# Kernel tuning notes

Measured on AMD Instinct MI355X. Metric: run time of the kernel, lower is better.

Reference implementation:

```python
import jax, jax.numpy as jnp
import numpy as np

B, T, S = 4, 128, 8192
HID, NH, NKV, HD = 2560, 8, 4, 256
INTER = 10240
WINDOW = 1024
SOFTCAP = 50.0
SCALING = 256 ** -0.5  # query_pre_attn_scalar ** -0.5
EPS = 1e-6
NEG = -2.3819763e38  # large negative for masking (matches Gemma mask value)
ROPE_THETA = 10000.0


def _rmsnorm(x, w):
    xf = x.astype(jnp.float32)
    o = xf * jax.lax.rsqrt(jnp.mean(xf * xf, axis=-1, keepdims=True) + EPS)
    return (o * (1.0 + w.astype(jnp.float32))).astype(x.dtype)


def _rope(x, cos, sin):
    # split-half rotation, matching torch apply_rotary_emb (chunk->complex->mul)
    d2 = x.shape[-1] // 2
    x1, x2 = x[..., :d2], x[..., d2:]
    c = cos[None, :, None, :]  # [1,T,1,D/2]
    s = sin[None, :, None, :]
    return jnp.concatenate([x1 * c - x2 * s, x1 * s + x2 * c], axis=-1)


def setup_inputs() -> dict:
    key = jax.random.key(0)
    ks = jax.random.split(key, 14)
    hidden_states = jax.random.normal(ks[0], (B, T, HID), jnp.float32)
    kv_write_indices = jnp.arange(T, dtype=jnp.int32)
    k_cache = jnp.zeros((B, S, NKV, HD), jnp.float32)
    v_cache = jnp.zeros((B, S, NKV, HD), jnp.float32)
    # rotary tables for positions 0..T-1
    inv = 1.0 / (ROPE_THETA ** (np.arange(0, HD, 2)[: HD // 2].astype(np.float32) / HD))
    fr = np.outer(np.arange(T, dtype=np.float32), inv).astype(np.float32)
    freqs_cos = jnp.asarray(np.cos(fr))
    freqs_sin = jnp.asarray(np.sin(fr))
    # masks: query i sits at absolute position i; cache slots >= T are unwritten
    qpos = jnp.arange(T)[:, None]
    kpos = jnp.arange(S)[None, :]
    causal = kpos <= qpos
    local = causal & ((qpos - kpos) < WINDOW)
    mask = jnp.broadcast_to(jnp.where(causal, 0.0, NEG)[None, None], (B, 1, T, S)).astype(jnp.float32)
    local_mask = jnp.broadcast_to(jnp.where(local, 0.0, NEG)[None, None], (B, 1, T, S)).astype(jnp.float32)
    sc = 0.02
    w_qkv = sc * jax.random.normal(ks[1], ((NH + 2 * NKV) * HD, HID), jnp.float32)
    w_o = sc * jax.random.normal(ks[2], (HID, NH * HD), jnp.float32)
    q_norm_w = 0.1 * jax.random.normal(ks[3], (HD,), jnp.float32)
    k_norm_w = 0.1 * jax.random.normal(ks[4], (HD,), jnp.float32)
    in_ln_w = 0.1 * jax.random.normal(ks[5], (HID,), jnp.float32)
    post_attn_ln_w = 0.1 * jax.random.normal(ks[6], (HID,), jnp.float32)
    pre_ffw_ln_w = 0.1 * jax.random.normal(ks[7], (HID,), jnp.float32)
    post_ffw_ln_w = 0.1 * jax.random.normal(ks[8], (HID,), jnp.float32)
    w_gate = sc * jax.random.normal(ks[9], (INTER, HID), jnp.float32)
    w_up = sc * jax.random.normal(ks[10], (INTER, HID), jnp.float32)
    w_down = sc * jax.random.normal(ks[11], (HID, INTER), jnp.float32)
    return {
        "hidden_states": hidden_states, "freqs_cos": freqs_cos, "freqs_sin": freqs_sin,
        "kv_write_indices": kv_write_indices, "k_cache": k_cache, "v_cache": v_cache,
        "mask": mask, "local_mask": local_mask,
        "w_qkv": w_qkv, "w_o": w_o, "q_norm_w": q_norm_w, "k_norm_w": k_norm_w,
        "in_ln_w": in_ln_w, "post_attn_ln_w": post_attn_ln_w,
        "pre_ffw_ln_w": pre_ffw_ln_w, "post_ffw_ln_w": post_ffw_ln_w,
        "w_gate": w_gate, "w_up": w_up, "w_down": w_down,
    }


def reference(hidden_states, freqs_cos, freqs_sin, kv_write_indices, k_cache, v_cache,
              mask, local_mask, w_qkv, w_o, q_norm_w, k_norm_w, in_ln_w,
              post_attn_ln_w, pre_ffw_ln_w, post_ffw_ln_w, w_gate, w_up, w_down):
    b, t, _ = hidden_states.shape
    residual = hidden_states
    h = _rmsnorm(hidden_states, in_ln_w)
    qkv = h @ w_qkv.T
    q_sz, kv_sz = NH * HD, NKV * HD
    xq = qkv[..., :q_sz].reshape(b, t, NH, HD)
    xk = qkv[..., q_sz:q_sz + kv_sz].reshape(b, t, NKV, HD)
    xv = qkv[..., q_sz + kv_sz:].reshape(b, t, NKV, HD)
    xq = _rmsnorm(xq, q_norm_w)  # QK-norm
    xk = _rmsnorm(xk, k_norm_w)
    xq = _rope(xq, freqs_cos, freqs_sin)
    xk = _rope(xk, freqs_cos, freqs_sin)
    kc = k_cache.at[:, kv_write_indices].set(xk)  # index_copy_ on dim 1
    vc = v_cache.at[:, kv_write_indices].set(xv)
    g = NH // NKV
    q = (xq * SCALING).reshape(b, t, NKV, g, HD)
    # GQA without repeat_interleave: group dim g shares each kv head
    scores = jnp.einsum('btkgd,bskd->bkgts', q, kc)
    scores = SOFTCAP * jnp.tanh(scores / SOFTCAP)  # logit softcapping
    scores = scores + local_mask[:, :, None]  # LOCAL_SLIDING -> use local mask
    probs = jax.nn.softmax(scores.astype(jnp.float32), axis=-1).astype(q.dtype)
    attn = jnp.einsum('bkgts,bskd->btkgd', probs, vc).reshape(b, t, NH * HD)
    attn = attn @ w_o.T
    h = residual + _rmsnorm(attn, post_attn_ln_w)
    residual = h
    x = _rmsnorm(h, pre_ffw_ln_w)
    gate = jax.nn.gelu(x @ w_gate.T, approximate=True)
    mlp = (gate * (x @ w_up.T)) @ w_down.T
    return residual + _rmsnorm(mlp, post_ffw_ln_w)
```

## Files before the change

### kernel.cpp

```cpp
#include <hip/hip_runtime.h>
#include <hip/hip_bf16.h>

#define B_ 4
#define T_ 128
#define HID 2560
#define NH 8
#define NKV 4
#define HD 256
#define INTER 10240
#define MROWS 512
#define EPS 1e-6f

typedef float f32x4 __attribute__((ext_vector_type(4)));
typedef __bf16 bf16x8 __attribute__((ext_vector_type(8)));

__device__ __forceinline__ unsigned short f2bf(float f){
  unsigned int u = __builtin_bit_cast(unsigned int, f);
  u += 0x7fffu + ((u >> 16) & 1u);
  return (unsigned short)(u >> 16);
}
__device__ __forceinline__ float bf2f(unsigned short u){
  unsigned int x = ((unsigned int)u) << 16;
  return __builtin_bit_cast(float, x);
}
__device__ __forceinline__ unsigned int cvtpk(float lo, float hi){
  unsigned int r;
  asm("v_cvt_pk_bf16_f32 %0, %1, %2" : "=v"(r) : "v"(lo), "v"(hi));
  return r;
}

__device__ __forceinline__ float bsum256(float v, float* buf){
  #pragma unroll
  for (int o = 32; o; o >>= 1) v += __shfl_xor(v, o);
  __syncthreads();
  if ((threadIdx.x & 63) == 0) buf[threadIdx.x >> 6] = v;
  __syncthreads();
  return buf[0] + buf[1] + buf[2] + buf[3];
}

__global__ __launch_bounds__(256) void rms_in(
    const float* __restrict__ x, const float* __restrict__ w,
    unsigned short* __restrict__ out)
{
  __shared__ float buf[4];
  const int r = blockIdx.x, tid = threadIdx.x;
  const float* xp = x + (size_t)r * HID;
  float v[10]; float ss = 0.f;
  #pragma unroll
  for (int j = 0; j < 10; j++){ v[j] = xp[tid + j*256]; ss += v[j]*v[j]; }
  ss = bsum256(ss, buf);
  float s = rsqrtf(ss * (1.f/HID) + EPS);
  #pragma unroll
  for (int j = 0; j < 10; j++){
    int i = tid + j*256;
    out[(size_t)r*HID + i] = f2bf(v[j] * s * (1.f + w[i]));
  }
}

template<bool BF16OUT>
__global__ __launch_bounds__(256, 2) void gemm_big(
    const unsigned short* __restrict__ A,
    const float* __restrict__ B0,
    const float* __restrict__ B1,
    int n_hi,
    void* __restrict__ Cv,
    int N, int K, int klen)
{
  __shared__ char As[2][256*64];
  __shared__ char Bs[2][128*64];
  const int tid = threadIdx.x;
  const int bid = (blockIdx.x & 7) * ((int)gridDim.x >> 3) + (blockIdx.x >> 3);
  const int bm = (bid & 1) << 8;
  const int bn = (bid >> 1) << 7;
  const int k0 = blockIdx.y * klen;
  const int nt = klen >> 5;

  const int srow = tid >> 1, shalf = tid & 1;
  const size_t A128 = (size_t)128 * K;
  const unsigned short* ApG = A + (size_t)(bm + srow) * K + k0 + (shalf << 4);
  const float* Bb = (bn < n_hi) ? B0 : B1;
  const int bnr = (bn < n_hi) ? bn : (bn - n_hi);
  const float* BpG = Bb + (size_t)(bnr + srow) * K + k0 + (shalf << 4);

  const int wave = tid >> 6, lane = tid & 63;
  const int wm = (wave & 1) << 7;
  const int wn = (wave >> 1) << 6;
  const int fr = lane & 15, kq = lane >> 4;
  const int aslot = ((kq ^ ((fr >> 1) & 3)) << 4);
  const int arsw = (srow >> 1) & 3;
  const int s0 = (((2*shalf)     ^ arsw) << 4);
  const int s1 = (((2*shalf + 1) ^ arsw) << 4);

  f32x4 acc[8][4];
  #pragma unroll
  for (int i = 0; i < 8; i++)
    #pragma unroll
    for (int j = 0; j < 4; j++)
      #pragma unroll
      for (int e = 0; e < 4; e++) acc[i][j][e] = 0.f;

  uint4 ra0, ra1, ra2, ra3; float4 rb0, rb1, rb2, rb3;
  uint4 sa0, sa1, sa2, sa3; float4 sb0, sb1, sb2, sb3;

#define LOAD_R(tt) { const unsigned short* ap = ApG + ((tt) << 5); const float* bp = BpG + ((tt) << 5); \
  ra0 = *(const uint4*)(ap); ra1 = *(const uint4*)(ap + 8); \
  ra2 = *(const uint4*)(ap + A128); ra3 = *(const uint4*)(ap + A128 + 8); \
  rb0 = *(const float4*)(bp); rb1 = *(const float4*)(bp + 4); \
  rb2 = *(const float4*)(bp + 8); rb3 = *(const float4*)(bp + 12); }
#define LOAD_S(tt) { const unsigned short* ap = ApG + ((tt) << 5); const float* bp = BpG + ((tt) << 5); \
  sa0 = *(const uint4*)(ap); sa1 = *(const uint4*)(ap + 8); \
  sa2 = *(const uint4*)(ap + A128); sa3 = *(const uint4*)(ap + A128 + 8); \
  sb0 = *(const float4*)(bp); sb1 = *(const float4*)(bp + 4); \
  sb2 = *(const float4*)(bp + 8); sb3 = *(const float4*)(bp + 12); }
#define WRITE_TILE(cur, a0,a1,a2,a3, b0,b1,b2,b3) { \
  char* abase = &As[cur][srow*64]; \
  *(uint4*)(abase + s0) = a0; \
  *(uint4*)(abase + s1) = a1; \
  *(uint4*)(abase + 128*64 + s0) = a2; \
  *(uint4*)(abase + 128*64 + s1) = a3; \
  uint4 w0, w1; \
  w0.x = cvtpk(b0.x,b0.y); w0.y = cvtpk(b0.z,b0.w); \
  w0.z = cvtpk(b1.x,b1.y); w0.w = cvtpk(b1.z,b1.w); \
  w1.x = cvtpk(b2.x,b2.y); w1.y = cvtpk(b2.z,b2.w); \
  w1.z = cvtpk(b3.x,b3.y); w1.w = cvtpk(b3.z,b3.w); \
  char* bbase = &Bs[cur][srow*64]; \
  *(uint4*)(bbase + s0) = w0; \
  *(uint4*)(bbase + s1) = w1; }

  auto COMPUTE = [&](int cur){
    const char* ab = As[cur];
    const char* bb = Bs[cur];
    bf16x8 af[8], bfv[4];
    #pragma unroll
    for (int mi = 0; mi < 8; mi++)
      af[mi] = *(const bf16x8*)(ab + ((wm + mi*16 + fr) << 6) + aslot);
    #pragma unroll
    for (int ni = 0; ni < 4; ni++)
      bfv[ni] = *(const bf16x8*)(bb + ((wn + ni*16 + fr) << 6) + aslot);
    __builtin_amdgcn_s_setprio(1);
    #pragma unroll
    for (int mi = 0; mi < 8; mi++)
      #pragma unroll
      for (int ni = 0; ni < 4; ni++)
        acc[mi][ni] = __builtin_amdgcn_mfma_f32_16x16x32_bf16(af[mi], bfv[ni], acc[mi][ni], 0, 0, 0);
    __builtin_amdgcn_s_setprio(0);
  };

  LOAD_R(0);
  LOAD_S(1);
  for (int t = 0; t < nt; t += 2) {
    WRITE_TILE(0, ra0,ra1,ra2,ra3, rb0,rb1,rb2,rb3);
    __syncthreads();
    if (t + 2 < nt) LOAD_R(t + 2);
    COMPUTE(0);
    WRITE_TILE(1, sa0,sa1,sa2,sa3, sb0,sb1,sb2,sb3);
    __syncthreads();
    if (t + 3 < nt) LOAD_S(t + 3);
    COMPUTE(1);
  }
#undef LOAD_R
#undef LOAD_S
#undef WRITE_TILE

  #pragma unroll
  for (int mi = 0; mi < 8; mi++) {
    #pragma unroll
    for (int ni = 0; ni < 4; ni++) {
      int m = bm + wm + mi*16 + kq*4;
      int n = bn + wn + ni*16 + fr;
      if (BF16OUT) {
        unsigned short* Cp = (unsigned short*)Cv + (size_t)blockIdx.y * MROWS * N;
        #pragma unroll
        for (int i = 0; i < 4; i++)
          Cp[(size_t)(m + i) * N + n] = f2bf(acc[mi][ni][i]);
      } else {
        float* Cp = (float*)Cv + (size_t)blockIdx.y * MROWS * N;
        #pragma unroll
        for (int i = 0; i < 4; i++)
          Cp[(size_t)(m + i) * N + n] = acc[mi][ni][i];
      }
    }
  }
}

__global__ __launch_bounds__(64) void qkv_post(
    const float* __restrict__ qkvp,
    const float* __restrict__ fcos, const float* __restrict__ fsin,
    const float* __restrict__ qnw, const float* __restrict__ knw,
    float* __restrict__ qout, float* __restrict__ kT, float* __restrict__ vout)
{
  const int row = blockIdx.x;
  const int hh  = blockIdx.y;
  const int b = row >> 7, t = row & 127;
  const int l = threadIdx.x;
  const size_t MS = (size_t)MROWS * 4096;
  const float* src = qkvp + (size_t)row * 4096 + hh * 256;
  float x[4];
  #pragma unroll
  for (int j = 0; j < 4; j++){
    int d = l + j*64;
    x[j] = src[d] + src[d + MS] + src[d + 2*MS] + src[d + 3*MS];
  }
  if (hh >= 12) {
    float* vp = vout + ((size_t)(b*NKV + (hh-12)) * T_ + t) * HD;
    #pragma unroll
    for (int j = 0; j < 4; j++) vp[l + j*64] = x[j];
    return;
  }
  float ss = x[0]*x[0] + x[1]*x[1] + x[2]*x[2] + x[3]*x[3];
  #pragma unroll
  for (int o = 32; o; o >>= 1) ss += __shfl_xor(ss, o);
  float r = rsqrtf(ss * (1.f/HD) + EPS);
  const float* nw = (hh < 8) ? qnw : knw;
  #pragma unroll
  for (int j = 0; j < 4; j++){ int d = l + j*64; x[j] = x[j] * r * (1.f + nw[d]); }
  float c0 = fcos[t*128 + l],      s0 = fsin[t*128 + l];
  float c1 = fcos[t*128 + l + 64], s1 = fsin[t*128 + l + 64];
  float y0 = x[0]*c0 - x[2]*s0;
  float y2 = x[0]*s0 + x[2]*c0;
  float y1 = x[1]*c1 - x[3]*s1;
  float y3 = x[1]*s1 + x[3]*c1;
  if (hh < 8) {
    float* qp = qout + ((size_t)(b*NH + hh) * T_ + t) * HD;
    const float sc = 0.0625f;
    qp[l] = y0*sc; qp[l+64] = y1*sc; qp[l+128] = y2*sc; qp[l+192] = y3*sc;
  } else {
    float* kp = kT + (size_t)(b*NKV + (hh-8)) * HD * T_;
    kp[(size_t)(l)*T_ + t] = y0;  kp[(size_t)(l+64)*T_ + t] = y1;
    kp[(size_t)(l+128)*T_ + t] = y2; kp[(size_t)(l+192)*T_ + t] = y3;
  }
}

__global__ __launch_bounds__(128) void attn_fwd(
    const float* __restrict__ q, const float* __restrict__ kT,
    const float* __restrict__ V, unsigned short* __restrict__ attn_out)
{
  const int id = blockIdx.x;
  const int t = id & 127;
  const int h = (id >> 7) & 7;
  const int b = id >> 10;
  const int kvh = h >> 1;
  const int tid = threadIdx.x;
  __shared__ float qs[256];
  __shared__ float sc[128];
  __shared__ float red[128];
  const float* qp = q + (size_t)id * HD;
  qs[tid] = qp[tid]; qs[tid + 128] = qp[tid + 128];
  __syncthreads();
  const float* kp = kT + (size_t)(b*NKV + kvh) * HD * T_;
  float dot = 0.f;
  const bool valid = (tid <= t);
  if (valid) {
    #pragma unroll 8
    for (int d = 0; d < 256; d++) dot += qs[d] * kp[(size_t)d*T_ + tid];
  }
  float score = valid ? 50.f * tanhf(dot * 0.02f) : -3.0e38f;
  sc[tid] = score; red[tid] = score;
  __syncthreads();
  for (int o = 64; o; o >>= 1){ if (tid < o) red[tid] = fmaxf(red[tid], red[tid+o]); __syncthreads(); }
  float m = red[0];
  __syncthreads();
  float p = valid ? __expf(score - m) : 0.f;
  sc[tid] = p; red[tid] = p;
  __syncthreads();
  for (int o = 64; o; o >>= 1){ if (tid < o) red[tid] += red[tid+o]; __syncthreads(); }
  float inv = 1.f / red[0];
  const float* vp = V + (size_t)(b*NKV + kvh) * T_ * HD;
  float a0 = 0.f, a1 = 0.f;
  for (int s = 0; s <= t; s++){
    float ps = sc[s];
    a0 += ps * vp[(size_t)s*HD + tid];
    a1 += ps * vp[(size_t)s*HD + tid + 128];
  }
  size_t orow = ((size_t)(b*T_ + t)) * 2048 + h * 256;
  attn_out[orow + tid]       = f2bf(a0 * inv);
  attn_out[orow + tid + 128] = f2bf(a1 * inv);
}

__global__ __launch_bounds__(256) void post_attn_k(
    const float* __restrict__ op, const float* __restrict__ hs,
    const float* __restrict__ wpost, const float* __restrict__ wpre,
    float* __restrict__ h2, unsigned short* __restrict__ xout)
{
  __shared__ float buf[4];
  const int r = blockIdx.x, tid = threadIdx.x;
  const size_t MS = (size_t)MROWS * HID;
  float o[10]; float ss = 0.f;
  #pragma unroll
  for (int j = 0; j < 10; j++){
    size_t i = (size_t)r*HID + tid + j*256;
    float v = 0.f;
    #pragma unroll
    for (int s = 0; s < 8; s++) v += op[i + s*MS];
    o[j] = v; ss += v*v;
  }
  ss = bsum256(ss, buf);
  float s = rsqrtf(ss*(1.f/HID) + EPS);
  float h[10]; float s2 = 0.f;
  #pragma unroll
  for (int j = 0; j < 10; j++){
    int i = tid + j*256;
    float hv = hs[(size_t)r*HID + i] + o[j]*s*(1.f + wpost[i]);
    h[j] = hv; h2[(size_t)r*HID + i] = hv; s2 += hv*hv;
  }
  s2 = bsum256(s2, buf);
  float sc2 = rsqrtf(s2*(1.f/HID) + EPS);
  #pragma unroll
  for (int j = 0; j < 10; j++){
    int i = tid + j*256;
    xout[(size_t)r*HID + i] = f2bf(h[j]*sc2*(1.f + wpre[i]));
  }
}

__global__ __launch_bounds__(256) void act_fuse(
    const unsigned short* __restrict__ gu,
    unsigned short* __restrict__ act)
{
  const int r = blockIdx.x;
  const size_t MS = (size_t)MROWS * 20480;
  const unsigned short* rowp = gu + (size_t)r * 20480;
  for (int c = threadIdx.x; c < INTER; c += 256){
    float g = 0.f, u = 0.f;
    #pragma unroll
    for (int s = 0; s < 4; s++){
      g += bf2f(rowp[s*MS + c]);
      u += bf2f(rowp[s*MS + c + INTER]);
    }
    float tt = tanhf(0.7978845608f * (g + 0.044715f * g*g*g));
    float ge = 0.5f * g * (1.f + tt);
    act[(size_t)r*INTER + c] = f2bf(ge * u);
  }
}

__global__ __launch_bounds__(256) void final_k(
    const float* __restrict__ dp, const float* __restrict__ h2,
    const float* __restrict__ w, float* __restrict__ out)
{
  __shared__ float buf[4];
  const int r = blockIdx.x, tid = threadIdx.x;
  const size_t MS = (size_t)MROWS * HID;
  float m[10]; float ss = 0.f;
  #pragma unroll
  for (int j = 0; j < 10; j++){
    size_t i = (size_t)r*HID + tid + j*256;
    float v = 0.f;
    #pragma unroll
    for (int s = 0; s < 8; s++) v += dp[i + s*MS];
    m[j] = v; ss += v*v;
  }
  ss = bsum256(ss, buf);
  float s = rsqrtf(ss*(1.f/HID) + EPS);
  #pragma unroll
  for (int j = 0; j < 10; j++){
    int i = tid + j*256;
    out[(size_t)r*HID + i] = h2[(size_t)r*HID + i] + m[j]*s*(1.f + w[i]);
  }
}

extern "C" void kernel_launch(void* const* d_in, const int* in_sizes, int n_in,
                              void* d_out, int out_size, void* d_ws, size_t ws_size,
                              hipStream_t stream)
{
  const float* hs     = (const float*)d_in[0];
  const float* fcos   = (const float*)d_in[1];
  const float* fsin   = (const float*)d_in[2];
  const float* w_qkv  = (const float*)d_in[8];
  const float* w_o    = (const float*)d_in[9];
  const float* qnw    = (const float*)d_in[10];
  const float* knw    = (const float*)d_in[11];
  const float* in_ln  = (const float*)d_in[12];
  const float* w_post = (const float*)d_in[13];
  const float* w_pre  = (const float*)d_in[14];
  const float* w_pffw = (const float*)d_in[15];
  const float* w_gate = (const float*)d_in[16];
  const float* w_up   = (const float*)d_in[17];
  const float* w_down = (const float*)d_in[18];
  float* out = (float*)d_out;

  char* p = (char*)d_ws;
  auto alloc = [&](size_t bytes)->void*{ void* r = p; p += (bytes + 255) & ~(size_t)255; return r; };
  void* P0 = alloc((size_t)4*MROWS*20480*2);
  void* P1 = alloc((size_t)8*MROWS*HID*4);
  unsigned short* h_b   = (unsigned short*)alloc((size_t)MROWS*HID*2);
  float* qbuf           = (float*)alloc((size_t)B_*NH*T_*HD*4);
  float* kT             = (float*)alloc((size_t)B_*NKV*HD*T_*4);
  float* vbuf           = (float*)alloc((size_t)B_*NKV*T_*HD*4);
  unsigned short* att_b = (unsigned short*)alloc((size_t)MROWS*2048*2);
  float* h2             = (float*)alloc((size_t)MROWS*HID*4);
  unsigned short* x_b   = (unsigned short*)alloc((size_t)MROWS*HID*2);
  unsigned short* act_b = (unsigned short*)alloc((size_t)MROWS*INTER*2);

  float* qkv_p          = (float*)P0;
  unsigned short* gu_p  = (unsigned short*)P0;
  float* o_p            = (float*)P1;
  float* down_p         = (float*)P1;

  rms_in<<<MROWS, 256, 0, stream>>>(hs, in_ln, h_b);
  gemm_big<false><<<dim3(64, 4), 256, 0, stream>>>(h_b, w_qkv, w_qkv, 1<<30, qkv_p, 4096, 2560, 640);
  qkv_post<<<dim3(MROWS, 16), 64, 0, stream>>>(qkv_p, fcos, fsin, qnw, knw, qbuf, kT, vbuf);
  attn_fwd<<<B_*NH*T_, 128, 0, stream>>>(qbuf, kT, vbuf, att_b);
  gemm_big<false><<<dim3(40, 8), 256, 0, stream>>>(att_b, w_o, w_o, 1<<30, o_p, 2560, 2048, 256);
  post_attn_k<<<MROWS, 256, 0, stream>>>(o_p, hs, w_post, w_pre, h2, x_b);
  gemm_big<true><<<dim3(320, 4), 256, 0, stream>>>(x_b, w_gate, w_up, 10240, gu_p, 20480, 2560, 640);
  act_fuse<<<MROWS, 256, 0, stream>>>(gu_p, act_b);
  gemm_big<false><<<dim3(40, 8), 256, 0, stream>>>(act_b, w_down, w_down, 1<<30, down_p, 2560, 10240, 1280);
  final_k<<<MROWS, 256, 0, stream>>>(down_p, h2, w_pffw, out);
}
```

Before: 369.7 us.

## Pre-tile activations into K-blocked layout and load A fragments directly to registers

Producers (rms_in, attn_fwd, post_attn_k, act_fuse) now write bf16 activations in a K-chunked [K/32][512][32] layout. The GEMM loads A fragments straight from global memory into registers, skipping the LDS staging and LDS reads for A; only B still goes through shared memory. Split-K counts are doubled for the QKV, O and down projections, and the reduction kernels and workspace grow to match. This adds more global A traffic per wave (no LDS reuse across waves) and more partial-sum reduction work in exchange for lower LDS pressure and higher grid parallelism.

```diff
diff --git a/kernel.cpp b/kernel.cpp
--- a/kernel.cpp
+++ b/kernel.cpp
@@ -38,6 +38,7 @@
   return buf[0] + buf[1] + buf[2] + buf[3];
 }
 
+
 __global__ __launch_bounds__(256) void rms_in(
     const float* __restrict__ x, const float* __restrict__ w,
     unsigned short* __restrict__ out)
@@ -53,43 +54,42 @@
   #pragma unroll
   for (int j = 0; j < 10; j++){
     int i = tid + j*256;
-    out[(size_t)r*HID + i] = f2bf(v[j] * s * (1.f + w[i]));
+    out[((size_t)(i >> 5) * MROWS + r) * 32 + (i & 31)] = f2bf(v[j] * s * (1.f + w[i]));
   }
 }
 
 template<bool BF16OUT>
 __global__ __launch_bounds__(256, 2) void gemm_big(
-    const unsigned short* __restrict__ A,
+    const unsigned short* __restrict__ Ap,
     const float* __restrict__ B0,
     const float* __restrict__ B1,
     int n_hi,
     void* __restrict__ Cv,
     int N, int K, int klen)
 {
-  __shared__ char As[2][256*64];
   __shared__ char Bs[2][128*64];
   const int tid = threadIdx.x;
   const int bid = (blockIdx.x & 7) * ((int)gridDim.x >> 3) + (blockIdx.x >> 3);
   const int bm = (bid & 1) << 8;
   const int bn = (bid >> 1) << 7;
-  const int k0 = blockIdx.y * klen;
+  const int kt0 = (blockIdx.y * klen) >> 5;
   const int nt = klen >> 5;
 
   const int srow = tid >> 1, shalf = tid & 1;
-  const size_t A128 = (size_t)128 * K;
-  const unsigned short* ApG = A + (size_t)(bm + srow) * K + k0 + (shalf << 4);
   const float* Bb = (bn < n_hi) ? B0 : B1;
   const int bnr = (bn < n_hi) ? bn : (bn - n_hi);
-  const float* BpG = Bb + (size_t)(bnr + srow) * K + k0 + (shalf << 4);
+  const float* BpG = Bb + (size_t)(bnr + srow) * K + (kt0 << 5) + (shalf << 4);
 
   const int wave = tid >> 6, lane = tid & 63;
   const int wm = (wave & 1) << 7;
   const int wn = (wave >> 1) << 6;
   const int fr = lane & 15, kq = lane >> 4;
-  const int aslot = ((kq ^ ((fr >> 1) & 3)) << 4);
-  const int arsw = (srow >> 1) & 3;
-  const int s0 = (((2*shalf)     ^ arsw) << 4);
-  const int s1 = (((2*shalf + 1) ^ arsw) << 4);
+  const int bslot = ((kq ^ ((fr >> 1) & 3)) << 4);
+  const int brsw = (srow >> 1) & 3;
+  const int s0 = (((2*shalf)     ^ brsw) << 4);
+  const int s1 = (((2*shalf + 1) ^ brsw) << 4);
+
+  const unsigned short* ApL = Ap + ((size_t)kt0 * MROWS + bm + wm + fr) * 32 + kq * 8;
 
   f32x4 acc[8][4];
   #pragma unroll
@@ -99,26 +99,18 @@
       #pragma unroll
       for (int e = 0; e < 4; e++) acc[i][j][e] = 0.f;
 
-  uint4 ra0, ra1, ra2, ra3; float4 rb0, rb1, rb2, rb3;
-  uint4 sa0, sa1, sa2, sa3; float4 sb0, sb1, sb2, sb3;
-
-#define LOAD_R(tt) { const unsigned short* ap = ApG + ((tt) << 5); const float* bp = BpG + ((tt) << 5); \
-  ra0 = *(const uint4*)(ap); ra1 = *(const uint4*)(ap + 8); \
-  ra2 = *(const uint4*)(ap + A128); ra3 = *(const uint4*)(ap + A128 + 8); \
-  rb0 = *(const float4*)(bp); rb1 = *(const float4*)(bp + 4); \
-  rb2 = *(const float4*)(bp + 8); rb3 = *(const float4*)(bp + 12); }
-#define LOAD_S(tt) { const unsigned short* ap = ApG + ((tt) << 5); const float* bp = BpG + ((tt) << 5); \
-  sa0 = *(const uint4*)(ap); sa1 = *(const uint4*)(ap + 8); \
-  sa2 = *(const uint4*)(ap + A128); sa3 = *(const uint4*)(ap + A128 + 8); \
-  sb0 = *(const float4*)(bp); sb1 = *(const float4*)(bp + 4); \
-  sb2 = *(const float4*)(bp + 8); sb3 = *(const float4*)(bp + 12); }
-#define WRITE_TILE(cur, a0,a1,a2,a3, b0,b1,b2,b3) { \
-  char* abase = &As[cur][srow*64]; \
-  *(uint4*)(abase + s0) = a0; \
-  *(uint4*)(abase + s1) = a1; \
-  *(uint4*)(abase + 128*64 + s0) = a2; \
-  *(uint4*)(abase + 128*64 + s1) = a3; \
-  uint4 w0, w1; \
+  uint4 aR[8], aS[8];
+  float4 rb0, rb1, rb2, rb3, sb0, sb1, sb2, sb3;
+
+#define ISSUE_A(dst, tt) { const unsigned short* ap = ApL + (size_t)(tt) * 16384; \
+  dst[0] = *(const uint4*)(ap);        dst[1] = *(const uint4*)(ap + 512); \
+  dst[2] = *(const uint4*)(ap + 1024); dst[3] = *(const uint4*)(ap + 1536); \
+  dst[4] = *(const uint4*)(ap + 2048); dst[5] = *(const uint4*)(ap + 2560); \
+  dst[6] = *(const uint4*)(ap + 3072); dst[7] = *(const uint4*)(ap + 3584); }
+#define LOAD_B(p0,p1,p2,p3, tt) { const float* bp = BpG + ((tt) << 5); \
+  p0 = *(const float4*)(bp);     p1 = *(const float4*)(bp + 4); \
+  p2 = *(const float4*)(bp + 8); p3 = *(const float4*)(bp + 12); }
+#define WRITE_B(cur, b0,b1,b2,b3) { uint4 w0, w1; \
   w0.x = cvtpk(b0.x,b0.y); w0.y = cvtpk(b0.z,b0.w); \
   w0.z = cvtpk(b1.x,b1.y); w0.w = cvtpk(b1.z,b1.w); \
   w1.x = cvtpk(b2.x,b2.y); w1.y = cvtpk(b2.z,b2.w); \
@@ -126,41 +118,37 @@
   char* bbase = &Bs[cur][srow*64]; \
   *(uint4*)(bbase + s0) = w0; \
   *(uint4*)(bbase + s1) = w1; }
-
-  auto COMPUTE = [&](int cur){
-    const char* ab = As[cur];
-    const char* bb = Bs[cur];
-    bf16x8 af[8], bfv[4];
-    #pragma unroll
-    for (int mi = 0; mi < 8; mi++)
-      af[mi] = *(const bf16x8*)(ab + ((wm + mi*16 + fr) << 6) + aslot);
-    #pragma unroll
-    for (int ni = 0; ni < 4; ni++)
-      bfv[ni] = *(const bf16x8*)(bb + ((wn + ni*16 + fr) << 6) + aslot);
-    __builtin_amdgcn_s_setprio(1);
-    #pragma unroll
-    for (int mi = 0; mi < 8; mi++)
-      #pragma unroll
-      for (int ni = 0; ni < 4; ni++)
-        acc[mi][ni] = __builtin_amdgcn_mfma_f32_16x16x32_bf16(af[mi], bfv[ni], acc[mi][ni], 0, 0, 0);
-    __builtin_amdgcn_s_setprio(0);
-  };
-
-  LOAD_R(0);
-  LOAD_S(1);
+#define COMPUTE(cur, aset) { const char* bb = Bs[cur]; \
+  bf16x8 bfv[4]; \
+  _Pragma("unroll") for (int ni = 0; ni < 4; ni++) \
+    bfv[ni] = *(const bf16x8*)(bb + ((wn + ni*16 + fr) << 6) + bslot); \
+  __builtin_amdgcn_s_setprio(1); \
+  _Pragma("unroll") for (int mi = 0; mi < 8; mi++){ \
+    bf16x8 af = __builtin_bit_cast(bf16x8, aset[mi]); \
+    _Pragma("unroll") for (int ni = 0; ni < 4; ni++) \
+      acc[mi][ni] = __builtin_amdgcn_mfma_f32_16x16x32_bf16(af, bfv[ni], acc[mi][ni], 0, 0, 0); } \
+  __builtin_amdgcn_s_setprio(0); }
+
+  ISSUE_A(aR, 0);
+  LOAD_B(rb0,rb1,rb2,rb3, 0);
+  LOAD_B(sb0,sb1,sb2,sb3, 1);
+
   for (int t = 0; t < nt; t += 2) {
-    WRITE_TILE(0, ra0,ra1,ra2,ra3, rb0,rb1,rb2,rb3);
+    WRITE_B(0, rb0,rb1,rb2,rb3);
     __syncthreads();
-    if (t + 2 < nt) LOAD_R(t + 2);
-    COMPUTE(0);
-    WRITE_TILE(1, sa0,sa1,sa2,sa3, sb0,sb1,sb2,sb3);
+    ISSUE_A(aS, t + 1);
+    if (t + 2 < nt) LOAD_B(rb0,rb1,rb2,rb3, t + 2);
+    COMPUTE(0, aR);
+    WRITE_B(1, sb0,sb1,sb2,sb3);
     __syncthreads();
-    if (t + 3 < nt) LOAD_S(t + 3);
-    COMPUTE(1);
-  }
-#undef LOAD_R
-#undef LOAD_S
-#undef WRITE_TILE
+    if (t + 2 < nt) ISSUE_A(aR, t + 2);
+    if (t + 3 < nt) LOAD_B(sb0,sb1,sb2,sb3, t + 3);
+    COMPUTE(1, aS);
+  }
+#undef ISSUE_A
+#undef LOAD_B
+#undef WRITE_B
+#undef COMPUTE
 
   #pragma unroll
   for (int mi = 0; mi < 8; mi++) {
@@ -199,7 +187,10 @@
   #pragma unroll
   for (int j = 0; j < 4; j++){
     int d = l + j*64;
-    x[j] = src[d] + src[d + MS] + src[d + 2*MS] + src[d + 3*MS];
+    float v = 0.f;
+    #pragma unroll
+    for (int s = 0; s < 8; s++) v += src[d + s*MS];
+    x[j] = v;
   }
   if (hh >= 12) {
     float* vp = vout + ((size_t)(b*NKV + (hh-12)) * T_ + t) * HD;
@@ -233,7 +224,7 @@
 
 __global__ __launch_bounds__(128) void attn_fwd(
     const float* __restrict__ q, const float* __restrict__ kT,
-    const float* __restrict__ V, unsigned short* __restrict__ attn_out)
+    const float* __restrict__ V, unsigned short* __restrict__ att)
 {
   const int id = blockIdx.x;
   const int t = id & 127;
@@ -272,9 +263,10 @@
     a0 += ps * vp[(size_t)s*HD + tid];
     a1 += ps * vp[(size_t)s*HD + tid + 128];
   }
-  size_t orow = ((size_t)(b*T_ + t)) * 2048 + h * 256;
-  attn_out[orow + tid]       = f2bf(a0 * inv);
-  attn_out[orow + tid + 128] = f2bf(a1 * inv);
+  const int row = b*T_ + t;
+  const int c0 = h*256 + tid, c1 = c0 + 128;
+  att[((size_t)(c0 >> 5) * MROWS + row) * 32 + (c0 & 31)] = f2bf(a0 * inv);
+  att[((size_t)(c1 >> 5) * MROWS + row) * 32 + (c1 & 31)] = f2bf(a1 * inv);
 }
 
 __global__ __launch_bounds__(256) void post_attn_k(
@@ -291,7 +283,7 @@
     size_t i = (size_t)r*HID + tid + j*256;
     float v = 0.f;
     #pragma unroll
-    for (int s = 0; s < 8; s++) v += op[i + s*MS];
+    for (int s = 0; s < 16; s++) v += op[i + s*MS];
     o[j] = v; ss += v*v;
   }
   ss = bsum256(ss, buf);
@@ -308,7 +300,7 @@
   #pragma unroll
   for (int j = 0; j < 10; j++){
     int i = tid + j*256;
-    xout[(size_t)r*HID + i] = f2bf(h[j]*sc2*(1.f + wpre[i]));
+    xout[((size_t)(i >> 5) * MROWS + r) * 32 + (i & 31)] = f2bf(h[j]*sc2*(1.f + wpre[i]));
   }
 }
 
@@ -328,7 +320,7 @@
     }
     float tt = tanhf(0.7978845608f * (g + 0.044715f * g*g*g));
     float ge = 0.5f * g * (1.f + tt);
-    act[(size_t)r*INTER + c] = f2bf(ge * u);
+    act[((size_t)(c >> 5) * MROWS + r) * 32 + (c & 31)] = f2bf(ge * u);
   }
 }
 
@@ -345,7 +337,7 @@
     size_t i = (size_t)r*HID + tid + j*256;
     float v = 0.f;
     #pragma unroll
-    for (int s = 0; s < 8; s++) v += dp[i + s*MS];
+    for (int s = 0; s < 16; s++) v += dp[i + s*MS];
     m[j] = v; ss += v*v;
   }
   ss = bsum256(ss, buf);
@@ -380,7 +372,7 @@
   char* p = (char*)d_ws;
   auto alloc = [&](size_t bytes)->void*{ void* r = p; p += (bytes + 255) & ~(size_t)255; return r; };
   void* P0 = alloc((size_t)4*MROWS*20480*2);
-  void* P1 = alloc((size_t)8*MROWS*HID*4);
+  void* P1 = alloc((size_t)16*MROWS*HID*4);
   unsigned short* h_b   = (unsigned short*)alloc((size_t)MROWS*HID*2);
   float* qbuf           = (float*)alloc((size_t)B_*NH*T_*HD*4);
   float* kT             = (float*)alloc((size_t)B_*NKV*HD*T_*4);
@@ -396,13 +388,13 @@
   float* down_p         = (float*)P1;
 
   rms_in<<<MROWS, 256, 0, stream>>>(hs, in_ln, h_b);
-  gemm_big<false><<<dim3(64, 4), 256, 0, stream>>>(h_b, w_qkv, w_qkv, 1<<30, qkv_p, 4096, 2560, 640);
+  gemm_big<false><<<dim3(64, 8), 256, 0, stream>>>(h_b, w_qkv, w_qkv, 1<<30, qkv_p, 4096, 2560, 320);
   qkv_post<<<dim3(MROWS, 16), 64, 0, stream>>>(qkv_p, fcos, fsin, qnw, knw, qbuf, kT, vbuf);
   attn_fwd<<<B_*NH*T_, 128, 0, stream>>>(qbuf, kT, vbuf, att_b);
-  gemm_big<false><<<dim3(40, 8), 256, 0, stream>>>(att_b, w_o, w_o, 1<<30, o_p, 2560, 2048, 256);
+  gemm_big<false><<<dim3(40, 16), 256, 0, stream>>>(att_b, w_o, w_o, 1<<30, o_p, 2560, 2048, 128);
   post_attn_k<<<MROWS, 256, 0, stream>>>(o_p, hs, w_post, w_pre, h2, x_b);
   gemm_big<true><<<dim3(320, 4), 256, 0, stream>>>(x_b, w_gate, w_up, 10240, gu_p, 20480, 2560, 640);
   act_fuse<<<MROWS, 256, 0, stream>>>(gu_p, act_b);
-  gemm_big<false><<<dim3(40, 8), 256, 0, stream>>>(act_b, w_down, w_down, 1<<30, down_p, 2560, 10240, 1280);
+  gemm_big<false><<<dim3(40, 16), 256, 0, stream>>>(act_b, w_down, w_down, 1<<30, down_p, 2560, 10240, 640);
   final_k<<<MROWS, 256, 0, stream>>>(down_p, h2, w_pffw, out);
 }
```

Result: faster. 357.2 us (-3.4%).
